# Optimization experiments

Hardware: AMD Instinct MI355X
Metric: run time of the kernel (lower is better)

The kernel has to match this reference:

```python
import jax, jax.numpy as jnp
import numpy as np
from jax import lax

B, T, D, L, H, F = 2, 128, 256, 8, 4, 2048  # batch, time, dim, max_chunk_len, nhead, dim_feedforward
THRESH = 0.5


def setup_inputs() -> dict:
    key = jax.random.key(0)
    ks = jax.random.split(key, 12)
    s = 0.02
    nrm = lambda k, sh, sc=s: jax.random.normal(k, sh, jnp.float32) * sc
    return {
        "frames": jax.random.normal(ks[0], (B, T, D), jnp.float32),
        "cls_token": jax.random.normal(ks[1], (D,), jnp.float32),
        "Wq": nrm(ks[2], (D, D)), "bq": jnp.zeros((D,), jnp.float32),
        "Wk": nrm(ks[3], (D, D)), "bk": jnp.zeros((D,), jnp.float32),
        "Wv": nrm(ks[4], (D, D)), "bv": jnp.zeros((D,), jnp.float32),
        "Wo": nrm(ks[5], (D, D)), "bo": jnp.zeros((D,), jnp.float32),
        "ln1_g": jnp.ones((D,), jnp.float32), "ln1_b": jnp.zeros((D,), jnp.float32),
        "ln2_g": jnp.ones((D,), jnp.float32), "ln2_b": jnp.zeros((D,), jnp.float32),
        "W1": nrm(ks[6], (D, F)), "b1f": jnp.zeros((F,), jnp.float32),
        "W2": nrm(ks[7], (F, D)), "b2f": jnp.zeros((D,), jnp.float32),
        "We1": nrm(ks[8], (D, D)), "be1": jnp.zeros((D,), jnp.float32),
        "We2": jax.random.normal(ks[9], (D,), jnp.float32) * 0.1,
        "be2": jnp.zeros((), jnp.float32),
    }


def reference(frames, cls_token, Wq, bq, Wk, bk, Wv, bv, Wo, bo,
              ln1_g, ln1_b, ln2_g, ln2_b, W1, b1f, W2, b2f,
              We1, be1, We2, be2):
    """Dynamic chunker: for each start index i, grow window 1..L over frames[i:],
    run a pre-norm TransformerEncoderLayer on [CLS, window], stop at first
    p_eoc > THRESH (or window cap). Emits CLS encodings per chunk.
    Returns (chunks [B,T,D] zero-padded, counts [B])."""
    Bq, Tq, Dq = frames.shape
    dh = Dq // H
    scale = 1.0 / np.sqrt(dh).astype(np.float32)

    def ln(x, g, b):
        m = jnp.mean(x, -1, keepdims=True)
        v = jnp.var(x, -1, keepdims=True)
        return (x - m) * lax.rsqrt(v + 1e-5) * g + b

    def enc_cls(seq, kp):
        # seq: (1+L, D); kp: (1+L,) True = padded key. norm_first encoder layer.
        S = seq.shape[0]
        h = ln(seq, ln1_g, ln1_b)
        q = (h @ Wq + bq).reshape(S, H, dh)
        k = (h @ Wk + bk).reshape(S, H, dh)
        v = (h @ Wv + bv).reshape(S, H, dh)
        scores = jnp.einsum('qhd,khd->hqk', q, k) * scale
        scores = jnp.where(kp[None, None, :], -1e30, scores)
        a = jax.nn.softmax(scores, axis=-1)
        o = jnp.einsum('hqk,khd->qhd', a, v).reshape(S, Dq)
        x = seq + o @ Wo + bo
        h2 = ln(x, ln2_g, ln2_b)
        x = x + jax.nn.relu(h2 @ W1 + b1f) @ W2 + b2f
        return x[0]  # CLS position

    pos = jnp.arange(L)
    ls = jnp.arange(1, L + 1)

    def run(fpad):  # fpad: (T+L, D), one sample
        def step(i, _):
            win = lax.dynamic_slice(fpad, (i, 0), (L, Dq))           # frames[i:i+L] (zero-padded past T)
            seq = jnp.concatenate([cls_token[None, :], win], 0)     # (1+L, D)
            base_pad = (i + pos) >= Tq                               # positions past end of sequence
            kp = jnp.concatenate(
                [jnp.zeros((L, 1), bool),
                 (pos[None, :] >= ls[:, None]) | base_pad[None, :]], 1)  # (L, 1+L) one mask per candidate len
            enc = jax.vmap(enc_cls, in_axes=(None, 0))(seq, kp)      # (L, D) candidate CLS encodings
            p = jax.nn.sigmoid(jax.nn.relu(enc @ We1 + be1) @ We2 + be2)  # (L,) eoc probs
            lmax = jnp.clip(Tq - i, 1, L)
            stop = (p > THRESH) & (ls <= lmax)
            lstar = jnp.where(stop.any(), jnp.argmax(stop) + 1, lmax)
            active = i < Tq
            chunk = jnp.where(active, enc[lstar - 1], jnp.zeros((Dq,), seq.dtype))
            i_new = jnp.where(active, i + lstar.astype(i.dtype), i)
            return i_new, (chunk, active)

        _, (chunks, act) = lax.scan(step, jnp.int32(0), None, length=Tq)
        return chunks, act

    fpadded = jnp.pad(frames, ((0, 0), (0, L), (0, 0)))
    chunks, act = jax.vmap(run)(fpadded)
    counts = act.sum(-1).astype(jnp.int32)
    return chunks, counts
```

## Files before the change

kernel.cpp:

```cpp
#include <hip/hip_runtime.h>

#define DEV __device__ __forceinline__

constexpr int Bc = 2, Tc = 128, Dc = 256, Lc = 8, Hc = 4, DH = 64, Fc = 2048;
constexpr float EPS = 1e-5f, SCALE = 0.125f;
constexpr int NROWS = Bc * Tc * Lc;
constexpr int SLAB = NROWS * Dc;

constexpr int OFF_K     = 0;
constexpr int OFF_VWOH  = OFF_K + Bc * Tc * Dc;
constexpr int OFF_QCLS  = OFF_VWOH + Bc * Tc * Hc * Dc;
constexpr int OFF_KCLS  = OFF_QCLS + Dc;
constexpr int OFF_VWOHC = OFF_KCLS + Dc;
constexpr int OFF_X0    = OFF_VWOHC + Hc * Dc;
constexpr int OFF_ENC   = OFF_X0;
constexpr int OFF_LNP   = OFF_X0 + SLAB;
constexpr int OFF_UP    = OFF_LNP + NROWS * 2;
constexpr int OFF_Z     = OFF_UP + 4 * SLAB;
constexpr int OFF_LST   = OFF_Z + NROWS;

DEV int imin(int a, int b) { return a < b ? a : b; }
DEV float4 f4add(float4 a, float4 b) {
  float4 r; r.x = a.x + b.x; r.y = a.y + b.y; r.z = a.z + b.z; r.w = a.w + b.w; return r;
}

DEV float blockReduceSum(float v, float* red) {
#pragma unroll
  for (int off = 32; off; off >>= 1) v += __shfl_down(v, off, 64);
  const int lane = threadIdx.x & 63;
  const int w = threadIdx.x >> 6;
  __syncthreads();
  if (lane == 0) red[w] = v;
  __syncthreads();
  return red[0] + red[1] + red[2] + red[3];
}

__global__ __launch_bounds__(256) void k_prep(
    const float* __restrict__ frames, const float* __restrict__ cls,
    const float* __restrict__ Wq, const float* __restrict__ bq,
    const float* __restrict__ Wk, const float* __restrict__ bk,
    const float* __restrict__ Wv, const float* __restrict__ bv,
    const float* __restrict__ Wo,
    const float* __restrict__ g1, const float* __restrict__ b1,
    float* __restrict__ ws) {
  __shared__ float hsm[Dc];
  __shared__ float vsm[Dc];
  __shared__ float red[4];
  const int d = threadIdx.x;
  const int r = blockIdx.x;

  const float x = (r < Bc * Tc) ? frames[r * Dc + d] : cls[d];
  const float s = blockReduceSum(x, red);
  const float m = s * (1.0f / Dc);
  const float c = x - m;
  const float var = blockReduceSum(c * c, red) * (1.0f / Dc);
  hsm[d] = c * (1.0f / sqrtf(var + EPS)) * g1[d] + b1[d];
  __syncthreads();

  float ka = bk[d], va = bv[d];
  for (int c2 = 0; c2 < Dc; ++c2) {
    const float h = hsm[c2];
    ka = fmaf(h, Wk[c2 * Dc + d], ka);
    va = fmaf(h, Wv[c2 * Dc + d], va);
  }
  if (r < Bc * Tc) ws[OFF_K + r * Dc + d] = ka;
  else             ws[OFF_KCLS + d] = ka;
  vsm[d] = va;
  __syncthreads();

#pragma unroll
  for (int hh = 0; hh < Hc; ++hh) {
    float acc = 0.f;
    for (int c2 = 0; c2 < DH; ++c2)
      acc = fmaf(vsm[hh * DH + c2], Wo[(hh * DH + c2) * Dc + d], acc);
    if (r < Bc * Tc) ws[OFF_VWOH + r * (Hc * Dc) + hh * Dc + d] = acc;
    else             ws[OFF_VWOHC + hh * Dc + d] = acc;
  }
  if (r == Bc * Tc) {
    float qa = bq[d];
    for (int c2 = 0; c2 < Dc; ++c2) qa = fmaf(hsm[c2], Wq[c2 * Dc + d], qa);
    ws[OFF_QCLS + d] = qa;
  }
}

__global__ __launch_bounds__(256) void k_attn(
    const float* __restrict__ cls, const float* __restrict__ bo,
    float* __restrict__ ws) {
  const int wg = blockIdx.x;
  const int i = wg & (Tc - 1);
  const int tid = threadIdx.x;
  const int wv = tid >> 6, lane = tid & 63;
  const int lmax = imin(Tc - i, Lc);
  __shared__ float sv[Hc][Lc + 1];
  __shared__ float aP[Lc][Hc][Lc + 1];
  __shared__ __align__(16) float redA[Lc][4];
  __shared__ __align__(16) float redB[Lc][4];

  {
    const float qv = ws[OFF_QCLS + wv * DH + lane];
    for (int j = 0; j <= Lc; ++j) {
      float p = 0.f;
      if (j == 0) p = qv * ws[OFF_KCLS + wv * DH + lane];
      else if (j - 1 < lmax) p = qv * ws[OFF_K + (wg + j - 1) * Dc + wv * DH + lane];
#pragma unroll
      for (int off = 32; off; off >>= 1) p += __shfl_down(p, off, 64);
      if (lane == 0) sv[wv][j] = p * SCALE;
    }
  }
  __syncthreads();

  if (tid < Lc * Hc) {
    const int l = (tid >> 2) + 1, h4 = tid & 3;
    if (l <= lmax) {
      float mx = -1e30f;
      for (int j = 0; j <= l; ++j) mx = fmaxf(mx, sv[h4][j]);
      float den = 0.f;
      for (int j = 0; j <= l; ++j) den += expf(sv[h4][j] - mx);
      const float inv = 1.f / den;
      for (int j = 0; j <= l; ++j) aP[l - 1][h4][j] = expf(sv[h4][j] - mx) * inv;
    }
  }
  __syncthreads();

  const int d = tid;
  float x0v[Lc];
  {
    const float base = cls[d] + bo[d];
#pragma unroll
    for (int l = 0; l < Lc; ++l) x0v[l] = base;
    for (int j = 0; j <= lmax; ++j) {
      const float* vwp = (j == 0) ? (ws + OFF_VWOHC)
                                  : (ws + OFF_VWOH + (wg + j - 1) * (Hc * Dc));
      for (int h4 = 0; h4 < Hc; ++h4) {
        const float w = vwp[h4 * Dc + d];
        const int lstart = (j == 0) ? 1 : j;
        for (int l = lstart; l <= lmax; ++l) x0v[l - 1] = fmaf(aP[l - 1][h4][j], w, x0v[l - 1]);
      }
    }
  }
#pragma unroll
  for (int l = 0; l < Lc; ++l) {
    float p = x0v[l];
#pragma unroll
    for (int off = 32; off; off >>= 1) p += __shfl_down(p, off, 64);
    if (lane == 0) redA[l][wv] = p;
  }
  __syncthreads();
  float mean[Lc];
#pragma unroll
  for (int l = 0; l < Lc; ++l) {
    const float4 s4 = *(const float4*)redA[l];
    mean[l] = (s4.x + s4.y + s4.z + s4.w) * (1.f / Dc);
  }
#pragma unroll
  for (int l = 0; l < Lc; ++l) {
    const float cv = x0v[l] - mean[l];
    float p = cv * cv;
#pragma unroll
    for (int off = 32; off; off >>= 1) p += __shfl_down(p, off, 64);
    if (lane == 0) redB[l][wv] = p;
  }
  __syncthreads();

  for (int l = 1; l <= Lc; ++l) {
    const int rowc = wg * Lc + l - 1;
    ws[OFF_X0 + rowc * Dc + d] = (l <= lmax) ? x0v[l - 1] : 0.f;
    if (d == 0) {
      if (l <= lmax) {
        const float4 s4 = *(const float4*)redB[l - 1];
        const float var = (s4.x + s4.y + s4.z + s4.w) * (1.f / Dc);
        ws[OFF_LNP + rowc * 2 + 0] = mean[l - 1];
        ws[OFF_LNP + rowc * 2 + 1] = 1.f / sqrtf(var + EPS);
      } else {
        ws[OFF_LNP + rowc * 2 + 0] = 0.f;
        ws[OFF_LNP + rowc * 2 + 1] = 0.f;
      }
    }
  }
}

__global__ __launch_bounds__(256, 3) void k_ffn(
    const float* __restrict__ W1, const float* __restrict__ b1f,
    const float* __restrict__ W2, const float* __restrict__ g2,
    const float* __restrict__ b2, float* __restrict__ ws) {
  const int mtile = blockIdx.x >> 2;
  const int q = blockIdx.x & 3;
  const int r0 = mtile * 16;
  const int tid = threadIdx.x;
  const int wv = tid >> 6, lane = tid & 63;
  __shared__ __align__(16) float h2s[16][256];
  __shared__ __align__(16) float ts[16][512];

  {
    const float4* src = (const float4*)(ws + OFF_X0 + r0 * Dc);
    float4* dst = (float4*)&h2s[0][0];
#pragma unroll
    for (int k = 0; k < 4; ++k) {
      const int i4 = tid + k * 256;
      const int r = i4 >> 6;
      const int dd = (i4 & 63) * 4;
      const float m = ws[OFF_LNP + (r0 + r) * 2 + 0];
      const float rstd = ws[OFF_LNP + (r0 + r) * 2 + 1];
      const float4 x = src[i4];
      const float4 gg = *(const float4*)&g2[dd];
      const float4 bb = *(const float4*)&b2[dd];
      float4 h;
      h.x = (x.x - m) * rstd * gg.x + bb.x;
      h.y = (x.y - m) * rstd * gg.y + bb.y;
      h.z = (x.z - m) * rstd * gg.z + bb.z;
      h.w = (x.w - m) * rstd * gg.w + bb.w;
      dst[i4] = h;
    }
  }
  __syncthreads();

  const int rh = tid >> 7;
  const int fl = (tid & 127) * 4;
  const int fg = q * 512 + fl;
  float t[8][4];
  {
    const float4 bb = *(const float4*)&b1f[fg];
#pragma unroll
    for (int r = 0; r < 8; ++r) { t[r][0] = bb.x; t[r][1] = bb.y; t[r][2] = bb.z; t[r][3] = bb.w; }
  }
  for (int c = 0; c < Dc; c += 4) {
    float4 w1v[4];
#pragma unroll
    for (int k = 0; k < 4; ++k) w1v[k] = *(const float4*)&W1[(c + k) * Fc + fg];
#pragma unroll
    for (int r = 0; r < 8; ++r) {
      const float4 h = *(const float4*)&h2s[rh * 8 + r][c];
      const float hv[4] = {h.x, h.y, h.z, h.w};
#pragma unroll
      for (int k = 0; k < 4; ++k) {
        t[r][0] = fmaf(hv[k], w1v[k].x, t[r][0]);
        t[r][1] = fmaf(hv[k], w1v[k].y, t[r][1]);
        t[r][2] = fmaf(hv[k], w1v[k].z, t[r][2]);
        t[r][3] = fmaf(hv[k], w1v[k].w, t[r][3]);
      }
    }
  }
#pragma unroll
  for (int r = 0; r < 8; ++r) {
    float4 v;
    v.x = fmaxf(t[r][0], 0.f); v.y = fmaxf(t[r][1], 0.f);
    v.z = fmaxf(t[r][2], 0.f); v.w = fmaxf(t[r][3], 0.f);
    *(float4*)&ts[rh * 8 + r][fl] = v;
  }
  __syncthreads();

  const int d4 = lane * 4;
  float u[16][4];
#pragma unroll
  for (int r = 0; r < 16; ++r) { u[r][0] = 0.f; u[r][1] = 0.f; u[r][2] = 0.f; u[r][3] = 0.f; }
  for (int kk = 0; kk < 128; kk += 4) {
    const int kl = wv * 128 + kk;
    const int kg = q * 512 + kl;
    float4 w2v[4];
#pragma unroll
    for (int k = 0; k < 4; ++k) w2v[k] = *(const float4*)&W2[(kg + k) * Dc + d4];
#pragma unroll
    for (int r = 0; r < 16; ++r) {
      const float4 h = *(const float4*)&ts[r][kl];
      const float hv[4] = {h.x, h.y, h.z, h.w};
#pragma unroll
      for (int k = 0; k < 4; ++k) {
        u[r][0] = fmaf(hv[k], w2v[k].x, u[r][0]);
        u[r][1] = fmaf(hv[k], w2v[k].y, u[r][1]);
        u[r][2] = fmaf(hv[k], w2v[k].z, u[r][2]);
        u[r][3] = fmaf(hv[k], w2v[k].w, u[r][3]);
      }
    }
  }
  __syncthreads();

  float* redb = &ts[0][0];
  if (wv < 2) {
    float* slab = redb + wv * 4096;
#pragma unroll
    for (int r = 0; r < 16; ++r) {
      float4 v; v.x = u[r][0]; v.y = u[r][1]; v.z = u[r][2]; v.w = u[r][3];
      *(float4*)&slab[r * 256 + d4] = v;
    }
  }
  __syncthreads();
  if (wv >= 2) {
    float* slab = redb + (wv - 2) * 4096;
#pragma unroll
    for (int r = 0; r < 16; ++r) {
      float4 p = *(float4*)&slab[r * 256 + d4];
      p.x += u[r][0]; p.y += u[r][1]; p.z += u[r][2]; p.w += u[r][3];
      *(float4*)&slab[r * 256 + d4] = p;
    }
  }
  __syncthreads();
  {
    const float4* A4 = (const float4*)redb;
    const float4* B4 = A4 + 1024;
    float4* up4 = (float4*)(ws + OFF_UP + q * SLAB + r0 * Dc);
#pragma unroll
    for (int k = 0; k < 4; ++k) {
      const int i4 = tid + k * 256;
      up4[i4] = f4add(A4[i4], B4[i4]);
    }
  }
}

__global__ __launch_bounds__(256) void k_encz(
    const float* __restrict__ We1, const float* __restrict__ be1,
    const float* __restrict__ We2, const float* __restrict__ be2,
    const float* __restrict__ b2f, float* __restrict__ ws) {
  const int wg = blockIdx.x;
  const int f = threadIdx.x;
  const int lane = f & 63, wv = f >> 6;
  __shared__ float encs[8][Dc];
  __shared__ __align__(16) float zred[8][4];
  __shared__ float zs[8];
  const float bb = b2f[f];
#pragma unroll
  for (int r = 0; r < 8; ++r) {
    const int row = wg * Lc + r;
    const float e = ((((ws[OFF_X0 + row * Dc + f] +
                        ws[OFF_UP + 0 * SLAB + row * Dc + f]) +
                       ws[OFF_UP + 1 * SLAB + row * Dc + f]) +
                      ws[OFF_UP + 2 * SLAB + row * Dc + f]) +
                     ws[OFF_UP + 3 * SLAB + row * Dc + f]) + bb;
    ws[OFF_ENC + row * Dc + f] = e;
    encs[r][f] = e;
  }
  __syncthreads();

  float g[8];
  const float be1f = be1[f];
#pragma unroll
  for (int r = 0; r < 8; ++r) g[r] = be1f;
  for (int c = 0; c < Dc; ++c) {
    const float w = We1[c * Dc + f];
#pragma unroll
    for (int r = 0; r < 8; ++r) g[r] = fmaf(encs[r][c], w, g[r]);
  }
  const float w2 = We2[f];
#pragma unroll
  for (int r = 0; r < 8; ++r) {
    float p = fmaxf(g[r], 0.f) * w2;
#pragma unroll
    for (int off = 32; off; off >>= 1) p += __shfl_down(p, off, 64);
    if (lane == 0) zred[r][wv] = p;
  }
  __syncthreads();
  if (f < 8) {
    const float4 s4 = *(const float4*)zred[f];
    zs[f] = s4.x + s4.y + s4.z + s4.w + be2[0];
    ws[OFF_Z + wg * Lc + f] = zs[f];
  }
  __syncthreads();
  if (f == 0) {
    const int i = wg & (Tc - 1);
    const int lmax = imin(Tc - i, Lc);
    int ls = lmax;
    for (int l = 1; l <= lmax; ++l) {
      if (zs[l - 1] > 0.f) { ls = l; break; }
    }
    ((int*)(ws + OFF_LST))[wg] = ls;
  }
}

__global__ __launch_bounds__(256) void k_emit(float* __restrict__ ws, float* __restrict__ out) {
  const int b = blockIdx.x;
  const int tid = threadIdx.x;
  __shared__ int lst[Tc];
  __shared__ int path[Tc];
  __shared__ int cnt_s;
  const int* lsrc = (const int*)(ws + OFF_LST);
  if (tid < Tc) lst[tid] = lsrc[b * Tc + tid];
  __syncthreads();
  if (tid < 64) {
    const int a0 = lst[tid], a1 = lst[64 + tid];
    int cur = 0, s = 0;
    while (cur < Tc) {
      const int l = (cur < 64) ? __shfl(a0, cur, 64) : __shfl(a1, cur - 64, 64);
      if (tid == 0) path[s] = cur * Lc + l - 1;
      ++s;
      cur += l;
    }
    if (tid == 0) cnt_s = s;
  }
  __syncthreads();
  const int c = cnt_s;
  for (int s0 = 0; s0 < Tc; s0 += 8) {
    float v[8];
#pragma unroll
    for (int k = 0; k < 8; ++k) {
      const int s = s0 + k;
      v[k] = (s < c) ? ws[OFF_ENC + (b * Tc * Lc + path[s]) * Dc + tid] : 0.f;
    }
#pragma unroll
    for (int k = 0; k < 8; ++k) out[(b * Tc + s0 + k) * Dc + tid] = v[k];
  }
  if (tid == 0) out[Bc * Tc * Dc + b] = (float)c;
}

extern "C" void kernel_launch(void* const* d_in, const int* in_sizes, int n_in,
                              void* d_out, int out_size, void* d_ws, size_t ws_size,
                              hipStream_t stream) {
  const float* frames = (const float*)d_in[0];
  const float* cls    = (const float*)d_in[1];
  const float* Wq     = (const float*)d_in[2];
  const float* bq     = (const float*)d_in[3];
  const float* Wk     = (const float*)d_in[4];
  const float* bk     = (const float*)d_in[5];
  const float* Wv     = (const float*)d_in[6];
  const float* bv     = (const float*)d_in[7];
  const float* Wo     = (const float*)d_in[8];
  const float* bo     = (const float*)d_in[9];
  const float* g1     = (const float*)d_in[10];
  const float* b1     = (const float*)d_in[11];
  const float* g2     = (const float*)d_in[12];
  const float* b2     = (const float*)d_in[13];
  const float* W1     = (const float*)d_in[14];
  const float* b1f    = (const float*)d_in[15];
  const float* W2     = (const float*)d_in[16];
  const float* b2f    = (const float*)d_in[17];
  const float* We1    = (const float*)d_in[18];
  const float* be1    = (const float*)d_in[19];
  const float* We2    = (const float*)d_in[20];
  const float* be2    = (const float*)d_in[21];
  float* ws = (float*)d_ws;
  float* out = (float*)d_out;

  k_prep<<<Bc * Tc + 1, 256, 0, stream>>>(frames, cls, Wq, bq, Wk, bk, Wv, bv, Wo, g1, b1, ws);
  k_attn<<<Bc * Tc, 256, 0, stream>>>(cls, bo, ws);
  k_ffn<<<(NROWS / 16) * 4, 256, 0, stream>>>(W1, b1f, W2, g2, b2, ws);
  k_encz<<<Bc * Tc, 256, 0, stream>>>(We1, be1, We2, be2, b2f, ws);
  k_emit<<<Bc, 256, 0, stream>>>(ws, out);
}
```

Before: 248.6 us.

## Fuse EOC head into FFN kernel via last-block atomic counter; prefetch weights

Removes the separate k_encz launch. The last of the four FFN split-blocks per row tile, detected with an atomic counter zeroed in k_attn, sums the partials and computes the eoc probability head for 16 rows. The W1 and W2 inner loops now double-buffer weight loads to hide global latency, and launch bounds are relaxed from 3 to 2 waves per SIMD. This adds threadfence/atomic serialization and more registers per thread, which may lower occupancy.

```diff
diff --git a/kernel.cpp b/kernel.cpp
--- a/kernel.cpp
+++ b/kernel.cpp
@@ -18,6 +18,7 @@
 constexpr int OFF_UP    = OFF_LNP + NROWS * 2;
 constexpr int OFF_Z     = OFF_UP + 4 * SLAB;
 constexpr int OFF_LST   = OFF_Z + NROWS;
+constexpr int OFF_CNT   = OFF_LST + Bc * Tc;
 
 DEV int imin(int a, int b) { return a < b ? a : b; }
 DEV float4 f4add(float4 a, float4 b) {
@@ -96,6 +97,8 @@
   __shared__ __align__(16) float redA[Lc][4];
   __shared__ __align__(16) float redB[Lc][4];
 
+  if (tid == 0 && (wg & 1) == 0) ((int*)(ws + OFF_CNT))[wg >> 1] = 0;
+
   {
     const float qv = ws[OFF_QCLS + wv * DH + lane];
     for (int j = 0; j <= Lc; ++j) {
@@ -179,10 +182,13 @@
   }
 }
 
-__global__ __launch_bounds__(256, 3) void k_ffn(
+__global__ __launch_bounds__(256, 2) void k_ffn(
     const float* __restrict__ W1, const float* __restrict__ b1f,
     const float* __restrict__ W2, const float* __restrict__ g2,
-    const float* __restrict__ b2, float* __restrict__ ws) {
+    const float* __restrict__ b2, const float* __restrict__ b2f,
+    const float* __restrict__ We1, const float* __restrict__ be1,
+    const float* __restrict__ We2, const float* __restrict__ be2,
+    float* __restrict__ ws) {
   const int mtile = blockIdx.x >> 2;
   const int q = blockIdx.x & 3;
   const int r0 = mtile * 16;
@@ -190,6 +196,9 @@
   const int wv = tid >> 6, lane = tid & 63;
   __shared__ __align__(16) float h2s[16][256];
   __shared__ __align__(16) float ts[16][512];
+  __shared__ __align__(16) float zred[16][4];
+  __shared__ float zs[16];
+  __shared__ int tailflag;
 
   {
     const float4* src = (const float4*)(ws + OFF_X0 + r0 * Dc);
@@ -223,20 +232,39 @@
 #pragma unroll
     for (int r = 0; r < 8; ++r) { t[r][0] = bb.x; t[r][1] = bb.y; t[r][2] = bb.z; t[r][3] = bb.w; }
   }
-  for (int c = 0; c < Dc; c += 4) {
-    float4 w1v[4];
-#pragma unroll
-    for (int k = 0; k < 4; ++k) w1v[k] = *(const float4*)&W1[(c + k) * Fc + fg];
-#pragma unroll
-    for (int r = 0; r < 8; ++r) {
-      const float4 h = *(const float4*)&h2s[rh * 8 + r][c];
-      const float hv[4] = {h.x, h.y, h.z, h.w};
-#pragma unroll
-      for (int k = 0; k < 4; ++k) {
-        t[r][0] = fmaf(hv[k], w1v[k].x, t[r][0]);
-        t[r][1] = fmaf(hv[k], w1v[k].y, t[r][1]);
-        t[r][2] = fmaf(hv[k], w1v[k].z, t[r][2]);
-        t[r][3] = fmaf(hv[k], w1v[k].w, t[r][3]);
+  {
+    float4 wA[4], wB[4];
+#pragma unroll
+    for (int k = 0; k < 4; ++k) wA[k] = *(const float4*)&W1[k * Fc + fg];
+    for (int c = 0; c < Dc; c += 8) {
+#pragma unroll
+      for (int k = 0; k < 4; ++k) wB[k] = *(const float4*)&W1[(c + 4 + k) * Fc + fg];
+#pragma unroll
+      for (int r = 0; r < 8; ++r) {
+        const float4 h = *(const float4*)&h2s[rh * 8 + r][c];
+        const float hv[4] = {h.x, h.y, h.z, h.w};
+#pragma unroll
+        for (int k = 0; k < 4; ++k) {
+          t[r][0] = fmaf(hv[k], wA[k].x, t[r][0]);
+          t[r][1] = fmaf(hv[k], wA[k].y, t[r][1]);
+          t[r][2] = fmaf(hv[k], wA[k].z, t[r][2]);
+          t[r][3] = fmaf(hv[k], wA[k].w, t[r][3]);
+        }
+      }
+      const int cn = (c + 8 < Dc) ? c + 8 : 0;
+#pragma unroll
+      for (int k = 0; k < 4; ++k) wA[k] = *(const float4*)&W1[(cn + k) * Fc + fg];
+#pragma unroll
+      for (int r = 0; r < 8; ++r) {
+        const float4 h = *(const float4*)&h2s[rh * 8 + r][c + 4];
+        const float hv[4] = {h.x, h.y, h.z, h.w};
+#pragma unroll
+        for (int k = 0; k < 4; ++k) {
+          t[r][0] = fmaf(hv[k], wB[k].x, t[r][0]);
+          t[r][1] = fmaf(hv[k], wB[k].y, t[r][1]);
+          t[r][2] = fmaf(hv[k], wB[k].z, t[r][2]);
+          t[r][3] = fmaf(hv[k], wB[k].w, t[r][3]);
+        }
       }
     }
   }
@@ -253,22 +281,40 @@
   float u[16][4];
 #pragma unroll
   for (int r = 0; r < 16; ++r) { u[r][0] = 0.f; u[r][1] = 0.f; u[r][2] = 0.f; u[r][3] = 0.f; }
-  for (int kk = 0; kk < 128; kk += 4) {
-    const int kl = wv * 128 + kk;
-    const int kg = q * 512 + kl;
-    float4 w2v[4];
-#pragma unroll
-    for (int k = 0; k < 4; ++k) w2v[k] = *(const float4*)&W2[(kg + k) * Dc + d4];
-#pragma unroll
-    for (int r = 0; r < 16; ++r) {
-      const float4 h = *(const float4*)&ts[r][kl];
-      const float hv[4] = {h.x, h.y, h.z, h.w};
-#pragma unroll
-      for (int k = 0; k < 4; ++k) {
-        u[r][0] = fmaf(hv[k], w2v[k].x, u[r][0]);
-        u[r][1] = fmaf(hv[k], w2v[k].y, u[r][1]);
-        u[r][2] = fmaf(hv[k], w2v[k].z, u[r][2]);
-        u[r][3] = fmaf(hv[k], w2v[k].w, u[r][3]);
+  {
+    const int kb = q * 512 + wv * 128;
+    float4 vA[4], vB[4];
+#pragma unroll
+    for (int k = 0; k < 4; ++k) vA[k] = *(const float4*)&W2[(kb + k) * Dc + d4];
+    for (int kk = 0; kk < 128; kk += 8) {
+#pragma unroll
+      for (int k = 0; k < 4; ++k) vB[k] = *(const float4*)&W2[(kb + kk + 4 + k) * Dc + d4];
+#pragma unroll
+      for (int r = 0; r < 16; ++r) {
+        const float4 h = *(const float4*)&ts[r][wv * 128 + kk];
+        const float hv[4] = {h.x, h.y, h.z, h.w};
+#pragma unroll
+        for (int k = 0; k < 4; ++k) {
+          u[r][0] = fmaf(hv[k], vA[k].x, u[r][0]);
+          u[r][1] = fmaf(hv[k], vA[k].y, u[r][1]);
+          u[r][2] = fmaf(hv[k], vA[k].z, u[r][2]);
+          u[r][3] = fmaf(hv[k], vA[k].w, u[r][3]);
+        }
+      }
+      const int kn = (kk + 8 < 128) ? kk + 8 : 0;
+#pragma unroll
+      for (int k = 0; k < 4; ++k) vA[k] = *(const float4*)&W2[(kb + kn + k) * Dc + d4];
+#pragma unroll
+      for (int r = 0; r < 16; ++r) {
+        const float4 h = *(const float4*)&ts[r][wv * 128 + kk + 4];
+        const float hv[4] = {h.x, h.y, h.z, h.w};
+#pragma unroll
+        for (int k = 0; k < 4; ++k) {
+          u[r][0] = fmaf(hv[k], vB[k].x, u[r][0]);
+          u[r][1] = fmaf(hv[k], vB[k].y, u[r][1]);
+          u[r][2] = fmaf(hv[k], vB[k].z, u[r][2]);
+          u[r][3] = fmaf(hv[k], vB[k].w, u[r][3]);
+        }
       }
     }
   }
@@ -304,62 +350,74 @@
       up4[i4] = f4add(A4[i4], B4[i4]);
     }
   }
-}
-
-__global__ __launch_bounds__(256) void k_encz(
-    const float* __restrict__ We1, const float* __restrict__ be1,
-    const float* __restrict__ We2, const float* __restrict__ be2,
-    const float* __restrict__ b2f, float* __restrict__ ws) {
-  const int wg = blockIdx.x;
-  const int f = threadIdx.x;
-  const int lane = f & 63, wv = f >> 6;
-  __shared__ float encs[8][Dc];
-  __shared__ __align__(16) float zred[8][4];
-  __shared__ float zs[8];
-  const float bb = b2f[f];
-#pragma unroll
-  for (int r = 0; r < 8; ++r) {
-    const int row = wg * Lc + r;
-    const float e = ((((ws[OFF_X0 + row * Dc + f] +
-                        ws[OFF_UP + 0 * SLAB + row * Dc + f]) +
-                       ws[OFF_UP + 1 * SLAB + row * Dc + f]) +
-                      ws[OFF_UP + 2 * SLAB + row * Dc + f]) +
-                     ws[OFF_UP + 3 * SLAB + row * Dc + f]) + bb;
-    ws[OFF_ENC + row * Dc + f] = e;
-    encs[r][f] = e;
-  }
-  __syncthreads();
-
-  float g[8];
-  const float be1f = be1[f];
-#pragma unroll
-  for (int r = 0; r < 8; ++r) g[r] = be1f;
-  for (int c = 0; c < Dc; ++c) {
-    const float w = We1[c * Dc + f];
-#pragma unroll
-    for (int r = 0; r < 8; ++r) g[r] = fmaf(encs[r][c], w, g[r]);
-  }
-  const float w2 = We2[f];
-#pragma unroll
-  for (int r = 0; r < 8; ++r) {
-    float p = fmaxf(g[r], 0.f) * w2;
-#pragma unroll
-    for (int off = 32; off; off >>= 1) p += __shfl_down(p, off, 64);
-    if (lane == 0) zred[r][wv] = p;
-  }
-  __syncthreads();
-  if (f < 8) {
-    const float4 s4 = *(const float4*)zred[f];
-    zs[f] = s4.x + s4.y + s4.z + s4.w + be2[0];
-    ws[OFF_Z + wg * Lc + f] = zs[f];
-  }
-  __syncthreads();
-  if (f == 0) {
+
+  __syncthreads();
+  if (tid == 0) {
+    __threadfence();
+    const int old = atomicAdd(((int*)(ws + OFF_CNT)) + mtile, 1);
+    tailflag = (old == 3);
+  }
+  __syncthreads();
+  if (!tailflag) return;
+  __threadfence();
+
+  {
+    const float bbf = b2f[tid];
+#pragma unroll
+    for (int r = 0; r < 16; ++r) {
+      const int row = r0 + r;
+      const float e = ((((ws[OFF_X0 + row * Dc + tid] +
+                          ws[OFF_UP + 0 * SLAB + row * Dc + tid]) +
+                         ws[OFF_UP + 1 * SLAB + row * Dc + tid]) +
+                        ws[OFF_UP + 2 * SLAB + row * Dc + tid]) +
+                       ws[OFF_UP + 3 * SLAB + row * Dc + tid]) + bbf;
+      ws[OFF_ENC + row * Dc + tid] = e;
+      h2s[r][tid] = e;
+    }
+  }
+  __syncthreads();
+
+  {
+    float g[16];
+    const float be1f = be1[tid];
+#pragma unroll
+    for (int r = 0; r < 16; ++r) g[r] = be1f;
+    for (int c = 0; c < Dc; c += 4) {
+      float wc[4];
+#pragma unroll
+      for (int k = 0; k < 4; ++k) wc[k] = We1[(c + k) * Dc + tid];
+#pragma unroll
+      for (int r = 0; r < 16; ++r) {
+        const float4 h = *(const float4*)&h2s[r][c];
+        g[r] = fmaf(h.x, wc[0], g[r]);
+        g[r] = fmaf(h.y, wc[1], g[r]);
+        g[r] = fmaf(h.z, wc[2], g[r]);
+        g[r] = fmaf(h.w, wc[3], g[r]);
+      }
+    }
+    const float w2v = We2[tid];
+#pragma unroll
+    for (int r = 0; r < 16; ++r) {
+      float p = fmaxf(g[r], 0.f) * w2v;
+#pragma unroll
+      for (int off = 32; off; off >>= 1) p += __shfl_down(p, off, 64);
+      if (lane == 0) zred[r][wv] = p;
+    }
+  }
+  __syncthreads();
+  if (tid < 16) {
+    const float4 s4 = *(const float4*)zred[tid];
+    zs[tid] = s4.x + s4.y + s4.z + s4.w + be2[0];
+    ws[OFF_Z + r0 + tid] = zs[tid];
+  }
+  __syncthreads();
+  if (tid < 2) {
+    const int wg = 2 * mtile + tid;
     const int i = wg & (Tc - 1);
     const int lmax = imin(Tc - i, Lc);
     int ls = lmax;
     for (int l = 1; l <= lmax; ++l) {
-      if (zs[l - 1] > 0.f) { ls = l; break; }
+      if (zs[tid * 8 + l - 1] > 0.f) { ls = l; break; }
     }
     ((int*)(ws + OFF_LST))[wg] = ls;
   }
@@ -430,7 +488,6 @@
 
   k_prep<<<Bc * Tc + 1, 256, 0, stream>>>(frames, cls, Wq, bq, Wk, bk, Wv, bv, Wo, g1, b1, ws);
   k_attn<<<Bc * Tc, 256, 0, stream>>>(cls, bo, ws);
-  k_ffn<<<(NROWS / 16) * 4, 256, 0, stream>>>(W1, b1f, W2, g2, b2, ws);
-  k_encz<<<Bc * Tc, 256, 0, stream>>>(We1, be1, We2, be2, b2f, ws);
+  k_ffn<<<(NROWS / 16) * 4, 256, 0, stream>>>(W1, b1f, W2, g2, b2, b2f, We1, be1, We2, be2, ws);
   k_emit<<<Bc, 256, 0, stream>>>(ws, out);
 }
```

Measured after the change: 297.4 us. +19.6%, slower.
